# Kernel optimization log

Measured on AMD Instinct MI355X. Metric: run time of the kernel, lower is better.

Reference implementation:

```python
import math
import jax, jax.numpy as jnp
import numpy as np

B, Q, M = 4, 512, 8192
LOC_D, SENS_D, EMB_D = 8, 256, 512


def setup_inputs() -> dict:
    key = jax.random.key(0)
    ks = jax.random.split(key, 6)
    location = jax.random.normal(ks[0], (B, Q, LOC_D), dtype=jnp.float32)
    # sds must be positive (they are squared and logged); keep them away from 0
    location_sd = jax.random.uniform(ks[1], (B, Q, LOC_D), dtype=jnp.float32) * 0.9 + 0.1
    memory_locations = jax.random.normal(ks[2], (B, M, LOC_D), dtype=jnp.float32)
    memory_location_sds = jax.random.uniform(ks[3], (B, M, LOC_D), dtype=jnp.float32) * 0.9 + 0.1
    memory_senses = jax.random.normal(ks[4], (B, M, EMB_D), dtype=jnp.float32)
    # sensory_read_proj: Linear(embed_dim -> sensory_dim, bias=False)
    W_read = jax.random.normal(ks[5], (SENS_D, EMB_D), dtype=jnp.float32) / math.sqrt(EMB_D)
    return {
        "location": location,
        "location_sd": location_sd,
        "memory_locations": memory_locations,
        "memory_location_sds": memory_location_sds,
        "memory_senses": memory_senses,
        "W_read": W_read,
    }


def reference(location, location_sd, memory_locations, memory_location_sds, memory_senses, W_read):
    # BidirectionalMemory.read with match_threshold=None, detach_* True (stop_gradient)
    mem_loc = jax.lax.stop_gradient(memory_locations)
    mem_sd = jax.lax.stop_gradient(memory_location_sds)
    mem_sense = jax.lax.stop_gradient(memory_senses)

    # (B,Q,1,D) - (B,1,M,D) -> (B,Q,M,D)
    delta = location[:, :, None, :] - mem_loc[:, None, :, :]
    var = location_sd[:, :, None, :] ** 2 + mem_sd[:, None, :, :] ** 2
    d = delta.shape[-1]
    # -0.5 * sum((delta^2 / (var+eps))^2) - 0.5*log(2pi)*D - sum(log(var))
    log_aff = (
        -0.5 * jnp.sum((delta ** 2 / (var + 1e-8)) ** 2, axis=-1)
        - 0.5 * math.log(2.0 * math.pi) * d
        - jnp.sum(jnp.log(var), axis=-1)
    )  # (B,Q,M)
    weights = jax.nn.softmax(log_aff, axis=-1)  # (B,Q,M)
    pre_sense = jnp.einsum("bqm,bme->bqe", weights, mem_sense)  # (B,Q,EMB_D)
    sense = jnp.einsum("bqe,se->bqs", pre_sense, W_read)  # (B,Q,SENS_D)
    return sense
```

## Files before the change

kernel.cpp:

```cpp
#include <hip/hip_runtime.h>
#include <hip/hip_bf16.h>

#define BB 4
#define QQ 512
#define MM 8192
#define DD 8
#define EE 512
#define SS 256

using f32x4  = __attribute__((ext_vector_type(4))) float;
using bf16x8 = __attribute__((ext_vector_type(8))) short;

__device__ __forceinline__ unsigned short f2bf(float f) {
  union { float f; unsigned int u; } v; v.f = f;
  unsigned int r = v.u + 0x7fffu + ((v.u >> 16) & 1u);
  return (unsigned short)(r >> 16);
}

#define QT 2
#define K1_THREADS 512
#define K1_ITERS (MM / K1_THREADS)

__global__ __launch_bounds__(512) void k_aff(
    const float* __restrict__ loc, const float* __restrict__ locsd,
    const float* __restrict__ mloc, const float* __restrict__ msd,
    unsigned short* __restrict__ wts)
{
  const int blk = blockIdx.x;
  const int b  = blk / (QQ / QT);
  const int q0 = (blk % (QQ / QT)) * QT;
  const int t  = threadIdx.x;

  float lx[QT][DD], ls2[QT][DD];
#pragma unroll
  for (int qi = 0; qi < QT; ++qi)
#pragma unroll
    for (int d = 0; d < DD; ++d) {
      const int base = ((b * QQ) + q0 + qi) * DD + d;
      lx[qi][d] = loc[base];
      float s = locsd[base];
      ls2[qi][d] = s * s;
    }

  const float4* ml4 = reinterpret_cast<const float4*>(mloc + (size_t)b * MM * DD);
  const float4* ms4 = reinterpret_cast<const float4*>(msd  + (size_t)b * MM * DD);

  float la[QT][K1_ITERS];
  float mx[QT];
#pragma unroll
  for (int qi = 0; qi < QT; ++qi) mx[qi] = -3.4e38f;

#pragma unroll
  for (int i = 0; i < K1_ITERS; ++i) {
    const int m = i * K1_THREADS + t;
    float4 a0 = ml4[2 * m], a1 = ml4[2 * m + 1];
    float4 s0 = ms4[2 * m], s1 = ms4[2 * m + 1];
    float mlv[DD] = {a0.x, a0.y, a0.z, a0.w, a1.x, a1.y, a1.z, a1.w};
    float msv[DD] = {s0.x, s0.y, s0.z, s0.w, s1.x, s1.y, s1.z, s1.w};
    float ms2[DD];
#pragma unroll
    for (int d = 0; d < DD; ++d) ms2[d] = msv[d] * msv[d];
#pragma unroll
    for (int qi = 0; qi < QT; ++qi) {
      float ssum = 0.f, p = 1.f;
#pragma unroll
      for (int d = 0; d < DD; ++d) {
        float v  = ls2[qi][d] + ms2[d];
        float r  = __builtin_amdgcn_rcpf(v + 1e-8f);
        float dd0 = lx[qi][d] - mlv[d];
        float tt = dd0 * dd0 * r;
        ssum = __builtin_fmaf(tt, tt, ssum);
        p *= v;
      }
      float lav = -0.5f * ssum - __logf(p);
      la[qi][i] = lav;
      mx[qi] = fmaxf(mx[qi], lav);
    }
  }

  __shared__ float red[QT][8];
  const int wv = t >> 6;
#pragma unroll
  for (int qi = 0; qi < QT; ++qi)
#pragma unroll
    for (int off = 32; off; off >>= 1)
      mx[qi] = fmaxf(mx[qi], __shfl_xor(mx[qi], off, 64));
  if ((t & 63) == 0) { red[0][wv] = mx[0]; red[1][wv] = mx[1]; }
  __syncthreads();
#pragma unroll
  for (int qi = 0; qi < QT; ++qi) {
    float m2 = red[qi][0];
#pragma unroll
    for (int w = 1; w < 8; ++w) m2 = fmaxf(m2, red[qi][w]);
    mx[qi] = m2;
  }

  float sm[QT] = {0.f, 0.f};
#pragma unroll
  for (int i = 0; i < K1_ITERS; ++i)
#pragma unroll
    for (int qi = 0; qi < QT; ++qi) {
      float e = __expf(la[qi][i] - mx[qi]);
      la[qi][i] = e;
      sm[qi] += e;
    }
  __syncthreads();
#pragma unroll
  for (int qi = 0; qi < QT; ++qi)
#pragma unroll
    for (int off = 32; off; off >>= 1)
      sm[qi] += __shfl_xor(sm[qi], off, 64);
  if ((t & 63) == 0) { red[0][wv] = sm[0]; red[1][wv] = sm[1]; }
  __syncthreads();
  float inv[QT];
#pragma unroll
  for (int qi = 0; qi < QT; ++qi) {
    float s = 0.f;
#pragma unroll
    for (int w = 0; w < 8; ++w) s += red[qi][w];
    inv[qi] = 1.0f / s;
  }

#pragma unroll
  for (int i = 0; i < K1_ITERS; ++i) {
    const int m = i * K1_THREADS + t;
#pragma unroll
    for (int qi = 0; qi < QT; ++qi)
      wts[((size_t)(b * QQ + q0 + qi)) * MM + m] = f2bf(la[qi][i] * inv[qi]);
  }
}

#define P_BM 256
#define P_BN 128
#define P_BK 64

__global__ __launch_bounds__(512) void k_proj(
    const float* __restrict__ V, const float* __restrict__ W,
    unsigned short* __restrict__ projT)
{
  const int m0 = blockIdx.x * P_BN;
  const int b  = blockIdx.y;
  const int t  = threadIdx.x;
  const int lane = t & 63;
  const int wv = t >> 6;
  const int wr = wv >> 1;
  const int wc = wv & 1;

  __shared__ short lA[P_BM * P_BK];
  __shared__ short lB[P_BN * P_BK];

  f32x4 acc[4][4] = {};

  const float* Vp = V + (size_t)b * MM * EE;

  for (int k0 = 0; k0 < EE; k0 += P_BK) {
    __syncthreads();
#pragma unroll
    for (int j = 0; j < 8; ++j) {
      int e0 = (j * 512 + t) * 4;
      int row = e0 >> 6, k = e0 & 63;
      float4 src = *reinterpret_cast<const float4*>(&W[row * EE + k0 + k]);
      int idx = (row * P_BK + k) ^ ((row & 7) << 3);
      ushort4 dv; dv.x = f2bf(src.x); dv.y = f2bf(src.y); dv.z = f2bf(src.z); dv.w = f2bf(src.w);
      *reinterpret_cast<ushort4*>(&lA[idx]) = dv;
    }
#pragma unroll
    for (int j = 0; j < 4; ++j) {
      int e0 = (j * 512 + t) * 4;
      int row = e0 >> 6, k = e0 & 63;
      float4 src = *reinterpret_cast<const float4*>(&Vp[(size_t)(m0 + row) * EE + k0 + k]);
      int idx = (row * P_BK + k) ^ ((row & 7) << 3);
      ushort4 dv; dv.x = f2bf(src.x); dv.y = f2bf(src.y); dv.z = f2bf(src.z); dv.w = f2bf(src.w);
      *reinterpret_cast<ushort4*>(&lB[idx]) = dv;
    }
    __syncthreads();
#pragma unroll
    for (int kk = 0; kk < 2; ++kk) {
      const int kofs = kk * 32 + (lane >> 4) * 8;
      const int r15 = lane & 15;
      bf16x8 af[4], bfv[4];
#pragma unroll
      for (int mi = 0; mi < 4; ++mi) {
        int row = wr * 64 + mi * 16 + r15;
        af[mi] = *reinterpret_cast<const bf16x8*>(&lA[(row * P_BK + kofs) ^ ((row & 7) << 3)]);
      }
#pragma unroll
      for (int ni = 0; ni < 4; ++ni) {
        int row = wc * 64 + ni * 16 + r15;
        bfv[ni] = *reinterpret_cast<const bf16x8*>(&lB[(row * P_BK + kofs) ^ ((row & 7) << 3)]);
      }
#pragma unroll
      for (int mi = 0; mi < 4; ++mi)
#pragma unroll
        for (int ni = 0; ni < 4; ++ni)
          acc[mi][ni] = __builtin_amdgcn_mfma_f32_16x16x32_bf16(af[mi], bfv[ni], acc[mi][ni], 0, 0, 0);
    }
  }

  unsigned short* outp = projT + (size_t)b * SS * MM;
  const int fr = (lane >> 4) * 4;
  const int fc = lane & 15;
#pragma unroll
  for (int mi = 0; mi < 4; ++mi)
#pragma unroll
    for (int ni = 0; ni < 4; ++ni)
#pragma unroll
      for (int r = 0; r < 4; ++r) {
        int s = wr * 64 + mi * 16 + fr + r;
        int m = m0 + wc * 64 + ni * 16 + fc;
        outp[(size_t)s * MM + m] = f2bf(acc[mi][ni][r]);
      }
}

#define G_BM 128
#define G_BN 128
#define G_BK 64
#define G_KSPLIT 8

__global__ __launch_bounds__(256) void k_wgemm(
    const unsigned short* __restrict__ wts,
    const unsigned short* __restrict__ projT,
    float* __restrict__ out)
{
  const int tile = blockIdx.x;
  const int ks   = blockIdx.y;
  const int b    = blockIdx.z;
  const int q0 = (tile >> 1) * G_BM;
  const int s0 = (tile & 1) * G_BN;
  const int kbeg = ks * (MM / G_KSPLIT);
  const int t = threadIdx.x;
  const int lane = t & 63;
  const int wv = t >> 6;
  const int wr = wv >> 1, wc = wv & 1;

  __shared__ short lA[G_BM * G_BK];
  __shared__ short lB[G_BN * G_BK];

  f32x4 acc[4][4] = {};
  const unsigned short* A  = wts   + (size_t)b * QQ * MM;
  const unsigned short* Bp = projT + (size_t)b * SS * MM;

  for (int k0 = kbeg; k0 < kbeg + MM / G_KSPLIT; k0 += G_BK) {
    __syncthreads();
#pragma unroll
    for (int j = 0; j < 4; ++j) {
      int e0 = (j * 256 + t) * 8;
      int row = e0 >> 6, k = e0 & 63;
      uint4 src = *reinterpret_cast<const uint4*>(&A[(size_t)(q0 + row) * MM + k0 + k]);
      *reinterpret_cast<uint4*>(&lA[e0 ^ ((row & 7) << 3)]) = src;
    }
#pragma unroll
    for (int j = 0; j < 4; ++j) {
      int e0 = (j * 256 + t) * 8;
      int row = e0 >> 6, k = e0 & 63;
      uint4 src = *reinterpret_cast<const uint4*>(&Bp[(size_t)(s0 + row) * MM + k0 + k]);
      *reinterpret_cast<uint4*>(&lB[e0 ^ ((row & 7) << 3)]) = src;
    }
    __syncthreads();
#pragma unroll
    for (int kk = 0; kk < 2; ++kk) {
      const int kofs = kk * 32 + (lane >> 4) * 8;
      const int r15 = lane & 15;
      bf16x8 af[4], bfv[4];
#pragma unroll
      for (int mi = 0; mi < 4; ++mi) {
        int row = wr * 64 + mi * 16 + r15;
        af[mi] = *reinterpret_cast<const bf16x8*>(&lA[(row * G_BK + kofs) ^ ((row & 7) << 3)]);
      }
#pragma unroll
      for (int ni = 0; ni < 4; ++ni) {
        int row = wc * 64 + ni * 16 + r15;
        bfv[ni] = *reinterpret_cast<const bf16x8*>(&lB[(row * G_BK + kofs) ^ ((row & 7) << 3)]);
      }
#pragma unroll
      for (int mi = 0; mi < 4; ++mi)
#pragma unroll
        for (int ni = 0; ni < 4; ++ni)
          acc[mi][ni] = __builtin_amdgcn_mfma_f32_16x16x32_bf16(af[mi], bfv[ni], acc[mi][ni], 0, 0, 0);
    }
  }

  const int fr = (lane >> 4) * 4;
  const int fc = lane & 15;
#pragma unroll
  for (int mi = 0; mi < 4; ++mi)
#pragma unroll
    for (int ni = 0; ni < 4; ++ni)
#pragma unroll
      for (int r = 0; r < 4; ++r) {
        int q = q0 + wr * 64 + mi * 16 + fr + r;
        int s = s0 + wc * 64 + ni * 16 + fc;
        atomicAdd(&out[(size_t)(b * QQ + q) * SS + s], acc[mi][ni][r]);
      }
}


extern "C" void kernel_launch(void* const* d_in, const int* in_sizes, int n_in,
                              void* d_out, int out_size, void* d_ws, size_t ws_size,
                              hipStream_t stream) {
  const float* loc    = (const float*)d_in[0];
  const float* locsd  = (const float*)d_in[1];
  const float* mloc   = (const float*)d_in[2];
  const float* msd    = (const float*)d_in[3];
  const float* msense = (const float*)d_in[4];
  const float* wread  = (const float*)d_in[5];
  float* out = (float*)d_out;

  const size_t wts_bytes  = (size_t)BB * QQ * MM * 2;
  const size_t proj_bytes = (size_t)BB * SS * MM * 2;
  if (ws_size < wts_bytes + proj_bytes) return;

  unsigned short* wts   = (unsigned short*)d_ws;
  unsigned short* projT = (unsigned short*)((char*)d_ws + wts_bytes);

  hipMemsetAsync(d_out, 0, (size_t)out_size * sizeof(float), stream);

  hipLaunchKernelGGL(k_aff, dim3(BB * QQ / QT), dim3(K1_THREADS), 0, stream,
                     loc, locsd, mloc, msd, wts);
  hipLaunchKernelGGL(k_proj, dim3(MM / P_BN, BB), dim3(512), 0, stream,
                     msense, wread, projT);
  hipLaunchKernelGGL(k_wgemm, dim3(8, G_KSPLIT, BB), dim3(256), 0, stream,
                     wts, projT, out);
}
```

Measured before the change: 129.1 us.

## Defer softmax normalization, register-prefetch GEMM loads, retile projection and split-K

The affinity kernel now stores unnormalized log-affinities in shared memory instead of registers. It computes them in log2 space with a min-based shift, writes exp2 weights directly, and leaves the 1/sum factor to be applied in the GEMM epilogue. Both GEMM kernels gain register double-buffering, loading the next K tile from global memory while the current one is stored to LDS. The projection kernel is retiled to 128x128 blocks of 256 threads, and split-K for the weight GEMM rises from 8 to 16. The large shared array in k_aff (64KB) may limit occupancy, and the higher split doubles the atomic traffic on the output.

```diff
diff --git a/kernel.cpp b/kernel.cpp
--- a/kernel.cpp
+++ b/kernel.cpp
@@ -11,25 +11,30 @@
 using f32x4  = __attribute__((ext_vector_type(4))) float;
 using bf16x8 = __attribute__((ext_vector_type(8))) short;
 
-__device__ __forceinline__ unsigned short f2bf(float f) {
-  union { float f; unsigned int u; } v; v.f = f;
-  unsigned int r = v.u + 0x7fffu + ((v.u >> 16) & 1u);
-  return (unsigned short)(r >> 16);
+static __device__ __forceinline__ unsigned short f2bf(float f) {
+  union { __hip_bfloat16 h; unsigned short u; } v;
+  v.h = __float2bfloat16(f);
+  return v.u;
 }
 
 #define QT 2
-#define K1_THREADS 512
-#define K1_ITERS (MM / K1_THREADS)
+#define K1_T 512
+#define K1_I (MM / K1_T)
 
 __global__ __launch_bounds__(512) void k_aff(
     const float* __restrict__ loc, const float* __restrict__ locsd,
     const float* __restrict__ mloc, const float* __restrict__ msd,
-    unsigned short* __restrict__ wts)
+    unsigned short* __restrict__ wts, float* __restrict__ inv)
 {
+  __shared__ float la_s[QT * K1_I * K1_T];
+  __shared__ float red[QT][8];
+
   const int blk = blockIdx.x;
-  const int b  = blk / (QQ / QT);
-  const int q0 = (blk % (QQ / QT)) * QT;
-  const int t  = threadIdx.x;
+  const int b   = blk / (QQ / QT);
+  const int q0  = (blk % (QQ / QT)) * QT;
+  const int t   = threadIdx.x;
+  const int lane = t & 63;
+  const int wv   = t >> 6;
 
   float lx[QT][DD], ls2[QT][DD];
 #pragma unroll
@@ -39,20 +44,17 @@
       const int base = ((b * QQ) + q0 + qi) * DD + d;
       lx[qi][d] = loc[base];
       float s = locsd[base];
-      ls2[qi][d] = s * s;
+      ls2[qi][d] = __builtin_fmaf(s, s, 1e-8f);
     }
 
   const float4* ml4 = reinterpret_cast<const float4*>(mloc + (size_t)b * MM * DD);
   const float4* ms4 = reinterpret_cast<const float4*>(msd  + (size_t)b * MM * DD);
 
-  float la[QT][K1_ITERS];
-  float mx[QT];
-#pragma unroll
-  for (int qi = 0; qi < QT; ++qi) mx[qi] = -3.4e38f;
-
-#pragma unroll
-  for (int i = 0; i < K1_ITERS; ++i) {
-    const int m = i * K1_THREADS + t;
+  float mn[QT] = {3.4e38f, 3.4e38f};
+
+#pragma unroll
+  for (int i = 0; i < K1_I; ++i) {
+    const int m = i * K1_T + t;
     float4 a0 = ml4[2 * m], a1 = ml4[2 * m + 1];
     float4 s0 = ms4[2 * m], s1 = ms4[2 * m + 1];
     float mlv[DD] = {a0.x, a0.y, a0.z, a0.w, a1.x, a1.y, a1.z, a1.w};
@@ -66,114 +68,115 @@
 #pragma unroll
       for (int d = 0; d < DD; ++d) {
         float v  = ls2[qi][d] + ms2[d];
-        float r  = __builtin_amdgcn_rcpf(v + 1e-8f);
-        float dd0 = lx[qi][d] - mlv[d];
-        float tt = dd0 * dd0 * r;
+        float r  = __builtin_amdgcn_rcpf(v);
+        float dl = lx[qi][d] - mlv[d];
+        float d2 = dl * dl;
+        float tt = d2 * r;
         ssum = __builtin_fmaf(tt, tt, ssum);
         p *= v;
       }
-      float lav = -0.5f * ssum - __logf(p);
-      la[qi][i] = lav;
-      mx[qi] = fmaxf(mx[qi], lav);
-    }
-  }
-
-  __shared__ float red[QT][8];
-  const int wv = t >> 6;
+      float lavp = __builtin_fmaf(ssum, 0.72134752f, __builtin_amdgcn_logf(p));
+      mn[qi] = fminf(mn[qi], lavp);
+      la_s[(qi * K1_I + i) * K1_T + t] = lavp;
+    }
+  }
+
 #pragma unroll
   for (int qi = 0; qi < QT; ++qi)
 #pragma unroll
     for (int off = 32; off; off >>= 1)
-      mx[qi] = fmaxf(mx[qi], __shfl_xor(mx[qi], off, 64));
-  if ((t & 63) == 0) { red[0][wv] = mx[0]; red[1][wv] = mx[1]; }
+      mn[qi] = fminf(mn[qi], __shfl_xor(mn[qi], off, 64));
+  if (lane == 0) { red[0][wv] = mn[0]; red[1][wv] = mn[1]; }
   __syncthreads();
+  float mnb[QT];
 #pragma unroll
   for (int qi = 0; qi < QT; ++qi) {
     float m2 = red[qi][0];
 #pragma unroll
-    for (int w = 1; w < 8; ++w) m2 = fmaxf(m2, red[qi][w]);
-    mx[qi] = m2;
-  }
+    for (int w = 1; w < 8; ++w) m2 = fminf(m2, red[qi][w]);
+    mnb[qi] = m2;
+  }
+  __syncthreads();
 
   float sm[QT] = {0.f, 0.f};
 #pragma unroll
-  for (int i = 0; i < K1_ITERS; ++i)
+  for (int i = 0; i < K1_I; ++i) {
+    const int m = i * K1_T + t;
 #pragma unroll
     for (int qi = 0; qi < QT; ++qi) {
-      float e = __expf(la[qi][i] - mx[qi]);
-      la[qi][i] = e;
+      float lv = la_s[(qi * K1_I + i) * K1_T + t];
+      float e  = __builtin_amdgcn_exp2f(mnb[qi] - lv);
       sm[qi] += e;
-    }
-  __syncthreads();
+      wts[((size_t)(b * QQ + q0 + qi)) * MM + m] = f2bf(e);
+    }
+  }
 #pragma unroll
   for (int qi = 0; qi < QT; ++qi)
 #pragma unroll
     for (int off = 32; off; off >>= 1)
       sm[qi] += __shfl_xor(sm[qi], off, 64);
-  if ((t & 63) == 0) { red[0][wv] = sm[0]; red[1][wv] = sm[1]; }
+  if (lane == 0) { red[0][wv] = sm[0]; red[1][wv] = sm[1]; }
   __syncthreads();
-  float inv[QT];
-#pragma unroll
-  for (int qi = 0; qi < QT; ++qi) {
-    float s = 0.f;
-#pragma unroll
-    for (int w = 0; w < 8; ++w) s += red[qi][w];
-    inv[qi] = 1.0f / s;
-  }
-
-#pragma unroll
-  for (int i = 0; i < K1_ITERS; ++i) {
-    const int m = i * K1_THREADS + t;
-#pragma unroll
-    for (int qi = 0; qi < QT; ++qi)
-      wts[((size_t)(b * QQ + q0 + qi)) * MM + m] = f2bf(la[qi][i] * inv[qi]);
-  }
-}
-
-#define P_BM 256
-#define P_BN 128
-#define P_BK 64
-
-__global__ __launch_bounds__(512) void k_proj(
+  if (t == 0) {
+#pragma unroll
+    for (int qi = 0; qi < QT; ++qi) {
+      float s = 0.f;
+#pragma unroll
+      for (int w = 0; w < 8; ++w) s += red[qi][w];
+      inv[b * QQ + q0 + qi] = 1.0f / s;
+    }
+  }
+}
+
+__global__ __launch_bounds__(256) void k_proj(
     const float* __restrict__ V, const float* __restrict__ W,
     unsigned short* __restrict__ projT)
 {
-  const int m0 = blockIdx.x * P_BN;
-  const int b  = blockIdx.y;
-  const int t  = threadIdx.x;
-  const int lane = t & 63;
-  const int wv = t >> 6;
-  const int wr = wv >> 1;
-  const int wc = wv & 1;
-
-  __shared__ short lA[P_BM * P_BK];
-  __shared__ short lB[P_BN * P_BK];
+  const int m0 = blockIdx.x * 128;
+  const int s0 = blockIdx.y * 128;
+  const int b  = blockIdx.z;
+  const int t = threadIdx.x, lane = t & 63, wv = t >> 6;
+  const int wr = wv >> 1, wc = wv & 1;
+
+  __shared__ short lA[128 * 64];
+  __shared__ short lB[128 * 64];
 
   f32x4 acc[4][4] = {};
 
-  const float* Vp = V + (size_t)b * MM * EE;
-
-  for (int k0 = 0; k0 < EE; k0 += P_BK) {
+  const float* Wp = W + (size_t)s0 * EE;
+  const float* Vp = V + (size_t)b * MM * EE + (size_t)m0 * EE;
+
+  const int r0 = t >> 4;
+  const int c0 = (t & 15) * 4;
+  const int swz = (r0 & 7) << 3;
+
+  float4 ra[8], rb[8];
+
+#define P_LOADS(K0)                                                        \
+  _Pragma("unroll")                                                        \
+  for (int j = 0; j < 8; ++j) {                                            \
+    const int row = j * 16 + r0;                                           \
+    ra[j] = *reinterpret_cast<const float4*>(&Wp[(size_t)row * EE + (K0) + c0]); \
+    rb[j] = *reinterpret_cast<const float4*>(&Vp[(size_t)row * EE + (K0) + c0]); \
+  }
+
+  P_LOADS(0)
+
+  for (int ki = 0; ki < 8; ++ki) {
     __syncthreads();
 #pragma unroll
     for (int j = 0; j < 8; ++j) {
-      int e0 = (j * 512 + t) * 4;
-      int row = e0 >> 6, k = e0 & 63;
-      float4 src = *reinterpret_cast<const float4*>(&W[row * EE + k0 + k]);
-      int idx = (row * P_BK + k) ^ ((row & 7) << 3);
-      ushort4 dv; dv.x = f2bf(src.x); dv.y = f2bf(src.y); dv.z = f2bf(src.z); dv.w = f2bf(src.w);
-      *reinterpret_cast<ushort4*>(&lA[idx]) = dv;
-    }
-#pragma unroll
-    for (int j = 0; j < 4; ++j) {
-      int e0 = (j * 512 + t) * 4;
-      int row = e0 >> 6, k = e0 & 63;
-      float4 src = *reinterpret_cast<const float4*>(&Vp[(size_t)(m0 + row) * EE + k0 + k]);
-      int idx = (row * P_BK + k) ^ ((row & 7) << 3);
-      ushort4 dv; dv.x = f2bf(src.x); dv.y = f2bf(src.y); dv.z = f2bf(src.z); dv.w = f2bf(src.w);
-      *reinterpret_cast<ushort4*>(&lB[idx]) = dv;
-    }
+      const int row = j * 16 + r0;
+      const int idx = (row * 64 + c0) ^ swz;
+      ushort4 da, db;
+      da.x = f2bf(ra[j].x); da.y = f2bf(ra[j].y); da.z = f2bf(ra[j].z); da.w = f2bf(ra[j].w);
+      db.x = f2bf(rb[j].x); db.y = f2bf(rb[j].y); db.z = f2bf(rb[j].z); db.w = f2bf(rb[j].w);
+      *reinterpret_cast<ushort4*>(&lA[idx]) = da;
+      *reinterpret_cast<ushort4*>(&lB[idx]) = db;
+    }
+    if (ki < 7) { P_LOADS((ki + 1) * 64) }
     __syncthreads();
+
 #pragma unroll
     for (int kk = 0; kk < 2; ++kk) {
       const int kofs = kk * 32 + (lane >> 4) * 8;
@@ -182,12 +185,12 @@
 #pragma unroll
       for (int mi = 0; mi < 4; ++mi) {
         int row = wr * 64 + mi * 16 + r15;
-        af[mi] = *reinterpret_cast<const bf16x8*>(&lA[(row * P_BK + kofs) ^ ((row & 7) << 3)]);
+        af[mi] = *reinterpret_cast<const bf16x8*>(&lA[(row * 64 + kofs) ^ ((row & 7) << 3)]);
       }
 #pragma unroll
       for (int ni = 0; ni < 4; ++ni) {
         int row = wc * 64 + ni * 16 + r15;
-        bfv[ni] = *reinterpret_cast<const bf16x8*>(&lB[(row * P_BK + kofs) ^ ((row & 7) << 3)]);
+        bfv[ni] = *reinterpret_cast<const bf16x8*>(&lB[(row * 64 + kofs) ^ ((row & 7) << 3)]);
       }
 #pragma unroll
       for (int mi = 0; mi < 4; ++mi)
@@ -196,6 +199,7 @@
           acc[mi][ni] = __builtin_amdgcn_mfma_f32_16x16x32_bf16(af[mi], bfv[ni], acc[mi][ni], 0, 0, 0);
     }
   }
+#undef P_LOADS
 
   unsigned short* outp = projT + (size_t)b * SS * MM;
   const int fr = (lane >> 4) * 4;
@@ -206,57 +210,64 @@
     for (int ni = 0; ni < 4; ++ni)
 #pragma unroll
       for (int r = 0; r < 4; ++r) {
-        int s = wr * 64 + mi * 16 + fr + r;
+        int s = s0 + wr * 64 + mi * 16 + fr + r;
         int m = m0 + wc * 64 + ni * 16 + fc;
         outp[(size_t)s * MM + m] = f2bf(acc[mi][ni][r]);
       }
 }
 
-#define G_BM 128
-#define G_BN 128
-#define G_BK 64
-#define G_KSPLIT 8
+#define KSPLIT 16
 
 __global__ __launch_bounds__(256) void k_wgemm(
     const unsigned short* __restrict__ wts,
     const unsigned short* __restrict__ projT,
+    const float* __restrict__ inv,
     float* __restrict__ out)
 {
   const int tile = blockIdx.x;
   const int ks   = blockIdx.y;
   const int b    = blockIdx.z;
-  const int q0 = (tile >> 1) * G_BM;
-  const int s0 = (tile & 1) * G_BN;
-  const int kbeg = ks * (MM / G_KSPLIT);
-  const int t = threadIdx.x;
-  const int lane = t & 63;
-  const int wv = t >> 6;
+  const int q0 = (tile >> 1) * 128;
+  const int s0 = (tile & 1) * 128;
+  const int kbeg = ks * (MM / KSPLIT);
+  const int t = threadIdx.x, lane = t & 63, wv = t >> 6;
   const int wr = wv >> 1, wc = wv & 1;
 
-  __shared__ short lA[G_BM * G_BK];
-  __shared__ short lB[G_BN * G_BK];
+  __shared__ short lA[128 * 64];
+  __shared__ short lB[128 * 64];
 
   f32x4 acc[4][4] = {};
-  const unsigned short* A  = wts   + (size_t)b * QQ * MM;
-  const unsigned short* Bp = projT + (size_t)b * SS * MM;
-
-  for (int k0 = kbeg; k0 < kbeg + MM / G_KSPLIT; k0 += G_BK) {
+  const unsigned short* A  = wts   + (size_t)b * QQ * MM + (size_t)q0 * MM;
+  const unsigned short* Bp = projT + (size_t)b * SS * MM + (size_t)s0 * MM;
+
+  const int r0 = t >> 3;
+  const int c0 = (t & 7) * 8;
+  const int swz = (r0 & 7) << 3;
+
+  uint4 ua[4], ub[4];
+
+#define G_LOADS(K0)                                                         \
+  _Pragma("unroll")                                                         \
+  for (int j = 0; j < 4; ++j) {                                             \
+    const int row = j * 32 + r0;                                            \
+    ua[j] = *reinterpret_cast<const uint4*>(&A[(size_t)row * MM + (K0) + c0]);  \
+    ub[j] = *reinterpret_cast<const uint4*>(&Bp[(size_t)row * MM + (K0) + c0]); \
+  }
+
+  G_LOADS(kbeg)
+
+  for (int ki = 0; ki < 8; ++ki) {
     __syncthreads();
 #pragma unroll
     for (int j = 0; j < 4; ++j) {
-      int e0 = (j * 256 + t) * 8;
-      int row = e0 >> 6, k = e0 & 63;
-      uint4 src = *reinterpret_cast<const uint4*>(&A[(size_t)(q0 + row) * MM + k0 + k]);
-      *reinterpret_cast<uint4*>(&lA[e0 ^ ((row & 7) << 3)]) = src;
-    }
-#pragma unroll
-    for (int j = 0; j < 4; ++j) {
-      int e0 = (j * 256 + t) * 8;
-      int row = e0 >> 6, k = e0 & 63;
-      uint4 src = *reinterpret_cast<const uint4*>(&Bp[(size_t)(s0 + row) * MM + k0 + k]);
-      *reinterpret_cast<uint4*>(&lB[e0 ^ ((row & 7) << 3)]) = src;
-    }
+      const int row = j * 32 + r0;
+      const int idx = (row * 64 + c0) ^ swz;
+      *reinterpret_cast<uint4*>(&lA[idx]) = ua[j];
+      *reinterpret_cast<uint4*>(&lB[idx]) = ub[j];
+    }
+    if (ki < 7) { G_LOADS(kbeg + (ki + 1) * 64) }
     __syncthreads();
+
 #pragma unroll
     for (int kk = 0; kk < 2; ++kk) {
       const int kofs = kk * 32 + (lane >> 4) * 8;
@@ -265,12 +276,12 @@
 #pragma unroll
       for (int mi = 0; mi < 4; ++mi) {
         int row = wr * 64 + mi * 16 + r15;
-        af[mi] = *reinterpret_cast<const bf16x8*>(&lA[(row * G_BK + kofs) ^ ((row & 7) << 3)]);
+        af[mi] = *reinterpret_cast<const bf16x8*>(&lA[(row * 64 + kofs) ^ ((row & 7) << 3)]);
       }
 #pragma unroll
       for (int ni = 0; ni < 4; ++ni) {
         int row = wc * 64 + ni * 16 + r15;
-        bfv[ni] = *reinterpret_cast<const bf16x8*>(&lB[(row * G_BK + kofs) ^ ((row & 7) << 3)]);
+        bfv[ni] = *reinterpret_cast<const bf16x8*>(&lB[(row * 64 + kofs) ^ ((row & 7) << 3)]);
       }
 #pragma unroll
       for (int mi = 0; mi < 4; ++mi)
@@ -279,19 +290,23 @@
           acc[mi][ni] = __builtin_amdgcn_mfma_f32_16x16x32_bf16(af[mi], bfv[ni], acc[mi][ni], 0, 0, 0);
     }
   }
+#undef G_LOADS
 
   const int fr = (lane >> 4) * 4;
   const int fc = lane & 15;
+  const float* invb = inv + b * QQ;
 #pragma unroll
   for (int mi = 0; mi < 4; ++mi)
 #pragma unroll
-    for (int ni = 0; ni < 4; ++ni)
-#pragma unroll
-      for (int r = 0; r < 4; ++r) {
-        int q = q0 + wr * 64 + mi * 16 + fr + r;
-        int s = s0 + wc * 64 + ni * 16 + fc;
-        atomicAdd(&out[(size_t)(b * QQ + q) * SS + s], acc[mi][ni][r]);
-      }
+    for (int r = 0; r < 4; ++r) {
+      const int q = q0 + wr * 64 + mi * 16 + fr + r;
+      const float iv = invb[q];
+#pragma unroll
+      for (int ni = 0; ni < 4; ++ni) {
+        const int s = s0 + wc * 64 + ni * 16 + fc;
+        atomicAdd(&out[(size_t)(b * QQ + q) * SS + s], acc[mi][ni][r] * iv);
+      }
+    }
 }
 
 
@@ -308,17 +323,19 @@
 
   const size_t wts_bytes  = (size_t)BB * QQ * MM * 2;
   const size_t proj_bytes = (size_t)BB * SS * MM * 2;
-  if (ws_size < wts_bytes + proj_bytes) return;
+  const size_t inv_bytes  = (size_t)BB * QQ * 4;
+  if (ws_size < wts_bytes + proj_bytes + inv_bytes) return;
 
   unsigned short* wts   = (unsigned short*)d_ws;
   unsigned short* projT = (unsigned short*)((char*)d_ws + wts_bytes);
+  float*          inv   = (float*)((char*)d_ws + wts_bytes + proj_bytes);
 
   hipMemsetAsync(d_out, 0, (size_t)out_size * sizeof(float), stream);
 
-  hipLaunchKernelGGL(k_aff, dim3(BB * QQ / QT), dim3(K1_THREADS), 0, stream,
-                     loc, locsd, mloc, msd, wts);
-  hipLaunchKernelGGL(k_proj, dim3(MM / P_BN, BB), dim3(512), 0, stream,
+  hipLaunchKernelGGL(k_aff, dim3(BB * QQ / QT), dim3(K1_T), 0, stream,
+                     loc, locsd, mloc, msd, wts, inv);
+  hipLaunchKernelGGL(k_proj, dim3(MM / 128, SS / 128, BB), dim3(256), 0, stream,
                      msense, wread, projT);
-  hipLaunchKernelGGL(k_wgemm, dim3(8, G_KSPLIT, BB), dim3(256), 0, stream,
-                     wts, projT, out);
-}
+  hipLaunchKernelGGL(k_wgemm, dim3(8, KSPLIT, BB), dim3(256), 0, stream,
+                     wts, projT, inv, out);
+}
```

Result: faster. 124.4 us (-3.7%).
